# Kernel optimization log

Hardware: AMD Instinct MI355X
Metric: run time of the kernel (lower is better)

Reference implementation:

```python
import jax, jax.numpy as jnp
import numpy as np

N, M, D, O = 16384, 4096, 256, 256

def setup_inputs() -> dict:
    key = jax.random.key(0)
    k1, k2, k3, k4, k5, k6, k7 = jax.random.split(key, 7)
    H_fine = jax.random.normal(k1, (N, D), dtype=jnp.float32)
    H_coarse = jax.random.normal(k2, (M, D), dtype=jnp.float32)
    inter_channel_adj = jax.random.randint(k3, (N, M), 0, 2).astype(jnp.float32)
    # attention = nn.Linear(2D, 1): weight vector [2D], bias scalar
    wa = jax.random.normal(k4, (2 * D,), dtype=jnp.float32) * (1.0 / np.sqrt(2 * D))
    ba = jax.random.normal(k5, (1,), dtype=jnp.float32) * 0.01
    # transform = nn.Linear(D, O), xavier_uniform weight
    lim = np.sqrt(6.0 / (D + O)).astype(np.float32)
    Wt = jax.random.uniform(k6, (O, D), minval=-lim, maxval=lim, dtype=jnp.float32)
    bt = jax.random.normal(k7, (O,), dtype=jnp.float32) * 0.01
    return {"H_fine": H_fine, "H_coarse": H_coarse,
            "inter_channel_adj": inter_channel_adj,
            "wa": wa, "ba": ba, "Wt": Wt, "bt": bt}

def reference(H_fine, H_coarse, inter_channel_adj, wa, ba, Wt, bt):
    d = H_fine.shape[-1]
    # additive attention: score_ij = [hf_i ; hc_j] . wa + b
    # = hf_i . wa[:d] + hc_j . wa[d:] + b  (avoids [N,M,2D] concat)
    sf = H_fine @ wa[:d]            # [N]
    sc = H_coarse @ wa[d:]          # [M]
    scores = sf[:, None] + sc[None, :] + ba[0]        # [N, M]
    masked = scores * inter_channel_adj               # [N, M]
    weights = jax.nn.softmax(masked, axis=-1)         # [N, M]
    attn_out = weights @ H_coarse                     # [N, D]
    attn_out = attn_out + H_fine                      # add_self=True
    out = attn_out @ Wt.T + bt                        # [N, O]
    return jax.nn.relu(out)
```

## Files before the change

kernel.cpp:

```cpp
#include <hip/hip_runtime.h>
#include <hip/hip_fp16.h>
#include <stdint.h>

#define N_ 16384
#define M_ 4096
#define D_ 256
#define O_ 256

#define WS_T    0
#define WS_U    65536
#define WS_R    81920
#define WS_WTP  98304
#define WS_BP   229376

typedef float  f32x4  __attribute__((ext_vector_type(4)));
typedef _Float16 half8 __attribute__((ext_vector_type(8)));

__device__ __forceinline__ unsigned short f2h(float f) {
  __half h = __float2half(f);
  unsigned short u;
  __builtin_memcpy(&u, &h, 2);
  return u;
}
__device__ __forceinline__ uint32_t hpack(float a, float b) {
  __half2 h = __floats2half2_rn(a, b);
  uint32_t u;
  __builtin_memcpy(&u, &h, 4);
  return u;
}

__global__ __launch_bounds__(256) void prep_kernel(
    const float* __restrict__ Hf, const float* __restrict__ Hc,
    const float* __restrict__ wa, const float* __restrict__ ba,
    const float* __restrict__ Wt, float* __restrict__ tv,
    float* __restrict__ uv, unsigned short* __restrict__ BP,
    unsigned short* __restrict__ WtP, float* __restrict__ Rv) {
  __shared__ float tile[64][65];
  __shared__ float red[4][64];
  int b = blockIdx.x;
  int t = threadIdx.x;
  if (b < 5120) {
    int wv = t >> 6, lane = t & 63;
    const float* X; const float* w; const float* bias; float* outv; int row;
    if (b < 4096) { X = Hf; w = wa;      bias = ba;      outv = tv; row = b * 4 + wv; }
    else          { X = Hc; w = wa + D_; bias = nullptr; outv = uv; row = (b - 4096) * 4 + wv; }
    const float4* x4 = (const float4*)(X + (size_t)row * D_);
    const float4* w4 = (const float4*)w;
    float4 xa = x4[lane], wa4 = w4[lane];
    float s = xa.x * wa4.x + xa.y * wa4.y + xa.z * wa4.z + xa.w * wa4.w;
#pragma unroll
    for (int off = 32; off > 0; off >>= 1) s += __shfl_xor(s, off);
    if (lane == 0) outv[row] = expf(s + (bias ? bias[0] : 0.0f));
  } else if (b < 5376) {
    int bb = b - 5120;
    int bk = bb >> 2;
    int bc = bb & 3;
    int k0 = bk * 64, col0 = bc * 64;
    int lane = t & 63, wv = t >> 6;
    int m = lane & 15, q = lane >> 4;
    float colsum = 0.0f;
#pragma unroll
    for (int i = 0; i < 16; ++i) {
      int e = t + 256 * i;
      int kk = e >> 6, cc = e & 63;
      float v = Hc[(size_t)(k0 + kk) * D_ + col0 + cc];
      tile[kk][cc] = v;
      colsum += v;
    }
    red[wv][t & 63] = colsum;
    __syncthreads();
    if (t < 64)
      atomicAdd(&Rv[col0 + t], red[0][t] + red[1][t] + red[2][t] + red[3][t]);
#pragma unroll
    for (int t8 = 0; t8 < 2; ++t8) {
      int tile_id = t8 * 4 + wv;
      int sub = tile_id >> 2, g = tile_id & 3;
      int kgg = bk * 2 + sub;
      int cgg = bc * 4 + g;
      unsigned short v8[8];
#pragma unroll
      for (int j = 0; j < 8; ++j)
        v8[j] = f2h(tile[sub * 32 + q * 8 + j][g * 16 + m]);
      *(uint4*)(BP + ((size_t)(kgg * 16 + cgg) * 64 + lane) * 8) = *(uint4*)v8;
    }
  } else {
    int tt = (b - 5376) * 256 + t;
    int lane = tt & 63, cg = (tt >> 6) & 15, kg = tt >> 10;
    int m = lane & 15, q = lane >> 4;
    const float* src = Wt + (size_t)(cg * 16 + m) * D_ + kg * 32 + q * 8;
    float4 w0 = *(const float4*)src, w1 = *(const float4*)(src + 4);
    unsigned short v8[8];
    v8[0] = f2h(w0.x); v8[1] = f2h(w0.y); v8[2] = f2h(w0.z); v8[3] = f2h(w0.w);
    v8[4] = f2h(w1.x); v8[5] = f2h(w1.y); v8[6] = f2h(w1.z); v8[7] = f2h(w1.w);
    *(uint4*)(WtP + (size_t)tt * 8) = *(uint4*)v8;
  }
}

__device__ __forceinline__ half8 frag_f16(uint32_t bits, __half2 th,
                                          const __half2* up, __half2 mone) {
  union { half8 h; uint32_t u[4]; } r;
#pragma unroll
  for (int p = 0; p < 4; ++p) {
    __half2 v = __hfma2(th, up[p], mone);
    uint32_t c;
    __builtin_memcpy(&c, &v, 4);
    uint32_t mlo = (uint32_t)((int32_t)(bits << (31 - 2 * p)) >> 31);
    uint32_t mhi = (uint32_t)((int32_t)(bits << (30 - 2 * p)) >> 31);
    r.u[p] = c & ((mlo & 0x0000FFFFu) | (mhi & 0xFFFF0000u));
  }
  return r.h;
}

#define COMPUTE_K(WB0, WB1, KK, BUF)                                          \
  {                                                                           \
    uint4 uu = *(const uint4*)&u_h2[(KK) * 16 + q * 4];                       \
    __half2 up[4];                                                            \
    __builtin_memcpy(up, &uu, 16);                                            \
    half8 af = frag_f16(((WB0) >> sh) & 0xffu, th0, up, mone);                \
    _Pragma("unroll")                                                         \
    for (int n = 0; n < 4; ++n)                                               \
      acc[0][n] = __builtin_amdgcn_mfma_f32_16x16x32_f16(af, BUF[n], acc[0][n], 0, 0, 0); \
    af = frag_f16(((WB1) >> sh) & 0xffu, th1, up, mone);                      \
    _Pragma("unroll")                                                         \
    for (int n = 0; n < 4; ++n)                                               \
      acc[1][n] = __builtin_amdgcn_mfma_f32_16x16x32_f16(af, BUF[n], acc[1][n], 0, 0, 0); \
  }

__global__ __launch_bounds__(512, 4) void mega_kernel(
    const float* __restrict__ adj, const unsigned short* __restrict__ BP,
    const float* __restrict__ tv, const float* __restrict__ uv,
    const float* __restrict__ Rv, const float* __restrict__ Hf,
    const unsigned short* __restrict__ WtP, const float* __restrict__ bt,
    float* __restrict__ out) {
  __shared__ __align__(16) char smem[74880];
  unsigned int (*bt2)[132] = (unsigned int (*)[132])(smem);
  float* u_lds = (float*)(smem + 16896);
  uint32_t* u_h2 = (uint32_t*)(smem + 33280);
  float (*Cred)[260] = (float (*)[260])(smem + 41472);
  float* Lsum_lds = (float*)(smem + 74752);
  unsigned short (*attn)[264] = (unsigned short (*)[264])(smem);

  int tid = threadIdx.x;
  int w = tid >> 6, lane = tid & 63;
  int q = lane >> 4, m = lane & 15;
  int colq = w >> 1, ksub = w & 1;
  int i0 = blockIdx.x * 32;

  for (int i = tid; i < M_ / 2; i += 512) {
    float2 u2 = *(const float2*)(uv + 2 * i);
    u_lds[2 * i] = u2.x; u_lds[2 * i + 1] = u2.y;
    u_h2[i] = hpack(u2.x, u2.y);
  }
  __syncthreads();

  {
    int r0 = w * 4;
    const float* ar = adj + ((size_t)i0 + r0) * M_;
    float su[4] = {0.f, 0.f, 0.f, 0.f}, sc[4] = {0.f, 0.f, 0.f, 0.f};
    float a[4][4], na[4][4];
#pragma unroll
    for (int j = 0; j < 4; ++j)
#pragma unroll
      for (int c = 0; c < 4; ++c)
        a[j][c] = ar[(size_t)j * M_ + c * 64 + lane];
#pragma unroll 1
    for (int i = 0; i < 16; ++i) {
      int k0 = i * 256;
      int k1 = (i + 1 < 16) ? k0 + 256 : 0;
#pragma unroll
      for (int j = 0; j < 4; ++j)
#pragma unroll
        for (int c = 0; c < 4; ++c)
          na[j][c] = ar[(size_t)j * M_ + k1 + c * 64 + lane];
      unsigned long long bal[4][4];
#pragma unroll
      for (int j = 0; j < 4; ++j) {
#pragma unroll
        for (int c = 0; c < 4; ++c) {
          bal[j][c] = __ballot(a[j][c] != 0.0f);
          su[j] = fmaf(a[j][c], u_lds[k0 + c * 64 + lane], su[j]);
        }
        sc[j] += (a[j][0] + a[j][1]) + (a[j][2] + a[j][3]);
      }
      if (lane < 32) {
        int rowsel = lane >> 3;
        int c = (lane >> 1) & 3, hi = lane & 1;
        unsigned long long v0 = (c == 0) ? bal[0][0] : (c == 1) ? bal[0][1] : (c == 2) ? bal[0][2] : bal[0][3];
        unsigned long long v1 = (c == 0) ? bal[1][0] : (c == 1) ? bal[1][1] : (c == 2) ? bal[1][2] : bal[1][3];
        unsigned long long v2 = (c == 0) ? bal[2][0] : (c == 1) ? bal[2][1] : (c == 2) ? bal[2][2] : bal[2][3];
        unsigned long long v3 = (c == 0) ? bal[3][0] : (c == 1) ? bal[3][1] : (c == 2) ? bal[3][2] : bal[3][3];
        unsigned long long v = (rowsel == 0) ? v0 : (rowsel == 1) ? v1 : (rowsel == 2) ? v2 : v3;
        bt2[r0 + rowsel][i * 8 + c * 2 + hi] =
            hi ? (unsigned int)(v >> 32) : (unsigned int)v;
      }
#pragma unroll
      for (int j = 0; j < 4; ++j)
#pragma unroll
        for (int c = 0; c < 4; ++c) a[j][c] = na[j][c];
    }
#pragma unroll
    for (int off = 32; off > 0; off >>= 1) {
#pragma unroll
      for (int j = 0; j < 4; ++j) {
        su[j] += __shfl_xor(su[j], off);
        sc[j] += __shfl_xor(sc[j], off);
      }
    }
    if (lane == 0) {
#pragma unroll
      for (int j = 0; j < 4; ++j)
        Lsum_lds[r0 + j] = tv[i0 + r0 + j] * su[j] - sc[j];
    }
  }

  const unsigned short* bbase = BP + (size_t)(colq * 4) * 512 + (size_t)lane * 8;
  int kg0 = ksub * 64;
  half8 bufA[4], bufB[4];
#pragma unroll
  for (int n = 0; n < 4; ++n)
    bufA[n] = *(const half8*)(bbase + ((size_t)kg0 * 16 + n) * 512);

  __half2 th0 = __float2half2_rn(tv[i0 + m]);
  __half2 th1 = __float2half2_rn(tv[i0 + 16 + m]);
  const __half2 mone = __float2half2_rn(-1.0f);

  f32x4 acc[2][4];
#pragma unroll
  for (int s = 0; s < 2; ++s)
#pragma unroll
    for (int n = 0; n < 4; ++n) acc[s][n] = (f32x4){0.f, 0.f, 0.f, 0.f};

  __syncthreads();

#pragma unroll 1
  for (int it2 = 0; it2 < 32; ++it2) {
    int kg = kg0 + it2 * 2;
    uint2 W0 = *(const uint2*)&bt2[m][kg];
    uint2 W1 = *(const uint2*)&bt2[16 + m][kg];
    int sh = q * 8;

#pragma unroll
    for (int n = 0; n < 4; ++n)
      bufB[n] = *(const half8*)(bbase + ((size_t)(kg + 1) * 16 + n) * 512);
    COMPUTE_K(W0.x, W1.x, kg, bufA)

    int kn = (it2 + 1 < 32) ? kg + 2 : kg0;
#pragma unroll
    for (int n = 0; n < 4; ++n)
      bufA[n] = *(const half8*)(bbase + ((size_t)kn * 16 + n) * 512);
    COMPUTE_K(W0.y, W1.y, kg + 1, bufB)
  }

#pragma unroll
  for (int s4 = 0; s4 < 2; ++s4) {
    if (ksub == s4) {
#pragma unroll
      for (int s = 0; s < 2; ++s)
#pragma unroll
        for (int n = 0; n < 4; ++n) {
          int col = colq * 64 + n * 16 + m;
#pragma unroll
          for (int r = 0; r < 4; ++r) {
            int rl = s * 16 + q * 4 + r;
            if (s4 == 0) Cred[rl][col] = acc[s][n][r];
            else         Cred[rl][col] += acc[s][n][r];
          }
        }
    }
    __syncthreads();
  }

  {
    int row = tid >> 4;
    int c0 = (tid & 15) * 16;
    size_t grow = (size_t)i0 + row;
    float invL = 1.0f / (Lsum_lds[row] + (float)M_);
    const float* hfp = Hf + grow * D_ + c0;
    const float* rvp = Rv + c0;
    const float* crp = &Cred[row][c0];
#pragma unroll
    for (int g = 0; g < 4; ++g) {
      float4 cv = *(const float4*)(crp + g * 4);
      float4 rv = *(const float4*)(rvp + g * 4);
      float4 hv = *(const float4*)(hfp + g * 4);
      float v0 = fmaf(cv.x + rv.x, invL, hv.x);
      float v1 = fmaf(cv.y + rv.y, invL, hv.y);
      float v2 = fmaf(cv.z + rv.z, invL, hv.z);
      float v3 = fmaf(cv.w + rv.w, invL, hv.w);
      *(uint32_t*)&attn[row][c0 + g * 4]     = hpack(v0, v1);
      *(uint32_t*)&attn[row][c0 + g * 4 + 2] = hpack(v2, v3);
    }
  }
  __syncthreads();

  {
    int rt = w & 1, cq = w >> 1;
    f32x4 facc[4];
#pragma unroll
    for (int n = 0; n < 4; ++n) facc[n] = (f32x4){0.f, 0.f, 0.f, 0.f};
    const unsigned short* wwave = WtP + (size_t)(cq * 4) * 512 + (size_t)lane * 8;
#pragma unroll
    for (int kf = 0; kf < 8; ++kf) {
      half8 af = *(const half8*)&attn[rt * 16 + m][kf * 32 + q * 8];
#pragma unroll
      for (int n = 0; n < 4; ++n) {
        half8 bf = *(const half8*)(wwave + ((size_t)kf * 16 + n) * 512);
        facc[n] = __builtin_amdgcn_mfma_f32_16x16x32_f16(af, bf, facc[n], 0, 0, 0);
      }
    }
#pragma unroll
    for (int n = 0; n < 4; ++n) {
      int col = cq * 64 + n * 16 + m;
      float b = bt[col];
#pragma unroll
      for (int r = 0; r < 4; ++r) {
        size_t row = (size_t)i0 + rt * 16 + q * 4 + r;
        out[row * O_ + col] = fmaxf(facc[n][r] + b, 0.0f);
      }
    }
  }
}

extern "C" void kernel_launch(void* const* d_in, const int* in_sizes, int n_in,
                              void* d_out, int out_size, void* d_ws, size_t ws_size,
                              hipStream_t stream) {
  const float* Hf  = (const float*)d_in[0];
  const float* Hc  = (const float*)d_in[1];
  const float* adj = (const float*)d_in[2];
  const float* wa  = (const float*)d_in[3];
  const float* ba  = (const float*)d_in[4];
  const float* Wt  = (const float*)d_in[5];
  const float* bt  = (const float*)d_in[6];
  float* out = (float*)d_out;

  char* ws = (char*)d_ws;
  float* tv   = (float*)(ws + WS_T);
  float* uv   = (float*)(ws + WS_U);
  float* Rv   = (float*)(ws + WS_R);
  unsigned short* WtP = (unsigned short*)(ws + WS_WTP);
  unsigned short* BP  = (unsigned short*)(ws + WS_BP);

  hipMemsetAsync(Rv, 0, D_ * sizeof(float), stream);

  prep_kernel<<<5408, 256, 0, stream>>>(Hf, Hc, wa, ba, Wt, tv, uv, BP, WtP, Rv);
  mega_kernel<<<512, 512, 0, stream>>>(adj, BP, tv, uv, Rv, Hf, WtP, bt, out);
}
```

Baseline: 441.5 us.

## Interleave adjacency bitmask streaming with MFMA chunks via double-buffered LDS bits

The adjacency scan and the masked MFMA accumulation used to run as two phases: all mask bits went to LDS first, then the GEMM ran. They now run as one 16-chunk software pipeline. Each iteration loads and ballots the next 256-column chunk of adj into a double-buffered LDS bitmask while computing MFMAs on the current chunk. The wave work split also changes: each wave now owns one 16-row tile and 8 column groups, with a K-split over 2 halves, instead of 2 row tiles and 4 column groups. This is meant to hide the HBM-bound adj read behind tensor-core work and to shrink LDS use. In exchange it adds a block-wide barrier per chunk and raises register pressure from 8 B fragments loaded per k-step.

Measured after the change: 430.9 us. -2.4%, faster.

```diff
diff --git a/kernel.cpp b/kernel.cpp
--- a/kernel.cpp
+++ b/kernel.cpp
@@ -111,19 +111,72 @@
   return r.h;
 }
 
-#define COMPUTE_K(WB0, WB1, KK, BUF)                                          \
+#define LOADS(KB)                                                             \
+  _Pragma("unroll")                                                           \
+  for (int cc = 0; cc < 4; ++cc) {                                            \
+    na0[cc] = ar[(size_t)0 * M_ + (KB) + cc * 64 + lane];                     \
+    na1[cc] = ar[(size_t)1 * M_ + (KB) + cc * 64 + lane];                     \
+    na2[cc] = ar[(size_t)2 * M_ + (KB) + cc * 64 + lane];                     \
+    na3[cc] = ar[(size_t)3 * M_ + (KB) + cc * 64 + lane];                     \
+  }
+
+#define TAIL(BUF, KB)                                                         \
   {                                                                           \
-    uint4 uu = *(const uint4*)&u_h2[(KK) * 16 + q * 4];                       \
+    unsigned long long bal0[4], bal1[4], bal2[4], bal3[4];                    \
+    _Pragma("unroll")                                                         \
+    for (int cc = 0; cc < 4; ++cc) {                                          \
+      float uvv = u_lds[(KB) + cc * 64 + lane];                               \
+      bal0[cc] = __ballot(na0[cc] != 0.0f);                                   \
+      bal1[cc] = __ballot(na1[cc] != 0.0f);                                   \
+      bal2[cc] = __ballot(na2[cc] != 0.0f);                                   \
+      bal3[cc] = __ballot(na3[cc] != 0.0f);                                   \
+      su[0] = fmaf(na0[cc], uvv, su[0]);                                      \
+      su[1] = fmaf(na1[cc], uvv, su[1]);                                      \
+      su[2] = fmaf(na2[cc], uvv, su[2]);                                      \
+      su[3] = fmaf(na3[cc], uvv, su[3]);                                      \
+    }                                                                         \
+    sc[0] += (na0[0] + na0[1]) + (na0[2] + na0[3]);                           \
+    sc[1] += (na1[0] + na1[1]) + (na1[2] + na1[3]);                           \
+    sc[2] += (na2[0] + na2[1]) + (na2[2] + na2[3]);                           \
+    sc[3] += (na3[0] + na3[1]) + (na3[2] + na3[3]);                           \
+    if (lane < 32) {                                                          \
+      int rowsel = lane >> 3, ccs = (lane >> 1) & 3, hi = lane & 1;           \
+      unsigned long long v0 = ccs == 0 ? bal0[0] : ccs == 1 ? bal0[1] : ccs == 2 ? bal0[2] : bal0[3]; \
+      unsigned long long v1 = ccs == 0 ? bal1[0] : ccs == 1 ? bal1[1] : ccs == 2 ? bal1[2] : bal1[3]; \
+      unsigned long long v2 = ccs == 0 ? bal2[0] : ccs == 1 ? bal2[1] : ccs == 2 ? bal2[2] : bal2[3]; \
+      unsigned long long v3 = ccs == 0 ? bal3[0] : ccs == 1 ? bal3[1] : ccs == 2 ? bal3[2] : bal3[3]; \
+      unsigned long long v = rowsel == 0 ? v0 : rowsel == 1 ? v1 : rowsel == 2 ? v2 : v3; \
+      bits_lds[BUF][w * 4 + rowsel][ccs * 2 + hi] =                           \
+          hi ? (unsigned int)(v >> 32) : (unsigned int)v;                     \
+    }                                                                         \
+  }
+
+#define COMPUTE(C, BUF)                                                       \
+  _Pragma("unroll")                                                           \
+  for (int kk = 0; kk < 4; ++kk) {                                            \
+    int kgc = ks * 4 + kk, kg = (C) * 8 + kgc;                                \
+    uint32_t b32 = bits_lds[BUF][rt * 16 + m][kgc];                           \
+    uint4 uu = *(const uint4*)&u_h2[kg * 16 + q * 4];                         \
+    const unsigned short* bp = BP + ((size_t)(kg * 16 + cgh * 8)) * 512 + (size_t)lane * 8; \
+    half8 bf0 = *(const half8*)(bp);                                          \
+    half8 bf1 = *(const half8*)(bp + 512);                                    \
+    half8 bf2 = *(const half8*)(bp + 1024);                                   \
+    half8 bf3 = *(const half8*)(bp + 1536);                                   \
+    half8 bf4 = *(const half8*)(bp + 2048);                                   \
+    half8 bf5 = *(const half8*)(bp + 2560);                                   \
+    half8 bf6 = *(const half8*)(bp + 3072);                                   \
+    half8 bf7 = *(const half8*)(bp + 3584);                                   \
     __half2 up[4];                                                            \
     __builtin_memcpy(up, &uu, 16);                                            \
-    half8 af = frag_f16(((WB0) >> sh) & 0xffu, th0, up, mone);                \
-    _Pragma("unroll")                                                         \
-    for (int n = 0; n < 4; ++n)                                               \
-      acc[0][n] = __builtin_amdgcn_mfma_f32_16x16x32_f16(af, BUF[n], acc[0][n], 0, 0, 0); \
-    af = frag_f16(((WB1) >> sh) & 0xffu, th1, up, mone);                      \
-    _Pragma("unroll")                                                         \
-    for (int n = 0; n < 4; ++n)                                               \
-      acc[1][n] = __builtin_amdgcn_mfma_f32_16x16x32_f16(af, BUF[n], acc[1][n], 0, 0, 0); \
+    half8 af = frag_f16((b32 >> sh) & 0xffu, th, up, mone);                   \
+    acc[0] = __builtin_amdgcn_mfma_f32_16x16x32_f16(af, bf0, acc[0], 0, 0, 0); \
+    acc[1] = __builtin_amdgcn_mfma_f32_16x16x32_f16(af, bf1, acc[1], 0, 0, 0); \
+    acc[2] = __builtin_amdgcn_mfma_f32_16x16x32_f16(af, bf2, acc[2], 0, 0, 0); \
+    acc[3] = __builtin_amdgcn_mfma_f32_16x16x32_f16(af, bf3, acc[3], 0, 0, 0); \
+    acc[4] = __builtin_amdgcn_mfma_f32_16x16x32_f16(af, bf4, acc[4], 0, 0, 0); \
+    acc[5] = __builtin_amdgcn_mfma_f32_16x16x32_f16(af, bf5, acc[5], 0, 0, 0); \
+    acc[6] = __builtin_amdgcn_mfma_f32_16x16x32_f16(af, bf6, acc[6], 0, 0, 0); \
+    acc[7] = __builtin_amdgcn_mfma_f32_16x16x32_f16(af, bf7, acc[7], 0, 0, 0); \
   }
 
 __global__ __launch_bounds__(512, 4) void mega_kernel(
@@ -132,140 +185,78 @@
     const float* __restrict__ Rv, const float* __restrict__ Hf,
     const unsigned short* __restrict__ WtP, const float* __restrict__ bt,
     float* __restrict__ out) {
-  __shared__ __align__(16) char smem[74880];
-  unsigned int (*bt2)[132] = (unsigned int (*)[132])(smem);
-  float* u_lds = (float*)(smem + 16896);
-  uint32_t* u_h2 = (uint32_t*)(smem + 33280);
-  float (*Cred)[260] = (float (*)[260])(smem + 41472);
-  float* Lsum_lds = (float*)(smem + 74752);
+  __shared__ __align__(16) char smem[60288];
+  unsigned int (*bits_lds)[32][9] = (unsigned int (*)[32][9])(smem);
+  float* u_lds = (float*)(smem + 2304);
+  uint32_t* u_h2 = (uint32_t*)(smem + 18688);
+  float (*Cred)[260] = (float (*)[260])(smem + 26880);
+  float* Lsum_lds = (float*)(smem + 60160);
   unsigned short (*attn)[264] = (unsigned short (*)[264])(smem);
 
   int tid = threadIdx.x;
   int w = tid >> 6, lane = tid & 63;
   int q = lane >> 4, m = lane & 15;
-  int colq = w >> 1, ksub = w & 1;
+  int rt = w & 1, cgh = (w >> 1) & 1, ks = w >> 2;
+  int sh = q * 8;
   int i0 = blockIdx.x * 32;
+
+  const float* ar = adj + ((size_t)i0 + w * 4) * M_;
+  float su[4] = {0.f, 0.f, 0.f, 0.f}, sc[4] = {0.f, 0.f, 0.f, 0.f};
+  float na0[4], na1[4], na2[4], na3[4];
+
+  LOADS(0)
 
   for (int i = tid; i < M_ / 2; i += 512) {
     float2 u2 = *(const float2*)(uv + 2 * i);
     u_lds[2 * i] = u2.x; u_lds[2 * i + 1] = u2.y;
     u_h2[i] = hpack(u2.x, u2.y);
   }
+
+  __half2 th = __float2half2_rn(tv[i0 + rt * 16 + m]);
+  const __half2 mone = __float2half2_rn(-1.0f);
+
+  f32x4 acc[8];
+#pragma unroll
+  for (int n = 0; n < 8; ++n) acc[n] = (f32x4){0.f, 0.f, 0.f, 0.f};
+
   __syncthreads();
-
-  {
-    int r0 = w * 4;
-    const float* ar = adj + ((size_t)i0 + r0) * M_;
-    float su[4] = {0.f, 0.f, 0.f, 0.f}, sc[4] = {0.f, 0.f, 0.f, 0.f};
-    float a[4][4], na[4][4];
+  TAIL(0, 0)
+  __syncthreads();
+
+#pragma unroll 1
+  for (int c = 0; c < 16; ++c) {
+    if (c < 15) { LOADS((c + 1) * 256) }
+    COMPUTE(c, c & 1)
+    if (c < 15) { TAIL((c + 1) & 1, (c + 1) * 256) }
+    __syncthreads();
+  }
+
+#pragma unroll
+  for (int off = 32; off > 0; off >>= 1) {
+    su[0] += __shfl_xor(su[0], off); sc[0] += __shfl_xor(sc[0], off);
+    su[1] += __shfl_xor(su[1], off); sc[1] += __shfl_xor(sc[1], off);
+    su[2] += __shfl_xor(su[2], off); sc[2] += __shfl_xor(sc[2], off);
+    su[3] += __shfl_xor(su[3], off); sc[3] += __shfl_xor(sc[3], off);
+  }
+  if (lane == 0) {
 #pragma unroll
     for (int j = 0; j < 4; ++j)
-#pragma unroll
-      for (int c = 0; c < 4; ++c)
-        a[j][c] = ar[(size_t)j * M_ + c * 64 + lane];
-#pragma unroll 1
-    for (int i = 0; i < 16; ++i) {
-      int k0 = i * 256;
-      int k1 = (i + 1 < 16) ? k0 + 256 : 0;
-#pragma unroll
-      for (int j = 0; j < 4; ++j)
-#pragma unroll
-        for (int c = 0; c < 4; ++c)
-          na[j][c] = ar[(size_t)j * M_ + k1 + c * 64 + lane];
-      unsigned long long bal[4][4];
-#pragma unroll
-      for (int j = 0; j < 4; ++j) {
-#pragma unroll
-        for (int c = 0; c < 4; ++c) {
-          bal[j][c] = __ballot(a[j][c] != 0.0f);
-          su[j] = fmaf(a[j][c], u_lds[k0 + c * 64 + lane], su[j]);
+      Lsum_lds[w * 4 + j] = tv[i0 + w * 4 + j] * su[j] - sc[j];
+  }
+
+#pragma unroll
+  for (int s4 = 0; s4 < 2; ++s4) {
+    if (ks == s4) {
+#pragma unroll
+      for (int g = 0; g < 8; ++g) {
+        int col = (cgh * 8 + g) * 16 + m;
+#pragma unroll
+        for (int r = 0; r < 4; ++r) {
+          int rl = rt * 16 + q * 4 + r;
+          if (s4 == 0) Cred[rl][col] = acc[g][r];
+          else         Cred[rl][col] += acc[g][r];
         }
-        sc[j] += (a[j][0] + a[j][1]) + (a[j][2] + a[j][3]);
       }
-      if (lane < 32) {
-        int rowsel = lane >> 3;
-        int c = (lane >> 1) & 3, hi = lane & 1;
-        unsigned long long v0 = (c == 0) ? bal[0][0] : (c == 1) ? bal[0][1] : (c == 2) ? bal[0][2] : bal[0][3];
-        unsigned long long v1 = (c == 0) ? bal[1][0] : (c == 1) ? bal[1][1] : (c == 2) ? bal[1][2] : bal[1][3];
-        unsigned long long v2 = (c == 0) ? bal[2][0] : (c == 1) ? bal[2][1] : (c == 2) ? bal[2][2] : bal[2][3];
-        unsigned long long v3 = (c == 0) ? bal[3][0] : (c == 1) ? bal[3][1] : (c == 2) ? bal[3][2] : bal[3][3];
-        unsigned long long v = (rowsel == 0) ? v0 : (rowsel == 1) ? v1 : (rowsel == 2) ? v2 : v3;
-        bt2[r0 + rowsel][i * 8 + c * 2 + hi] =
-            hi ? (unsigned int)(v >> 32) : (unsigned int)v;
-      }
-#pragma unroll
-      for (int j = 0; j < 4; ++j)
-#pragma unroll
-        for (int c = 0; c < 4; ++c) a[j][c] = na[j][c];
-    }
-#pragma unroll
-    for (int off = 32; off > 0; off >>= 1) {
-#pragma unroll
-      for (int j = 0; j < 4; ++j) {
-        su[j] += __shfl_xor(su[j], off);
-        sc[j] += __shfl_xor(sc[j], off);
-      }
-    }
-    if (lane == 0) {
-#pragma unroll
-      for (int j = 0; j < 4; ++j)
-        Lsum_lds[r0 + j] = tv[i0 + r0 + j] * su[j] - sc[j];
-    }
-  }
-
-  const unsigned short* bbase = BP + (size_t)(colq * 4) * 512 + (size_t)lane * 8;
-  int kg0 = ksub * 64;
-  half8 bufA[4], bufB[4];
-#pragma unroll
-  for (int n = 0; n < 4; ++n)
-    bufA[n] = *(const half8*)(bbase + ((size_t)kg0 * 16 + n) * 512);
-
-  __half2 th0 = __float2half2_rn(tv[i0 + m]);
-  __half2 th1 = __float2half2_rn(tv[i0 + 16 + m]);
-  const __half2 mone = __float2half2_rn(-1.0f);
-
-  f32x4 acc[2][4];
-#pragma unroll
-  for (int s = 0; s < 2; ++s)
-#pragma unroll
-    for (int n = 0; n < 4; ++n) acc[s][n] = (f32x4){0.f, 0.f, 0.f, 0.f};
-
-  __syncthreads();
-
-#pragma unroll 1
-  for (int it2 = 0; it2 < 32; ++it2) {
-    int kg = kg0 + it2 * 2;
-    uint2 W0 = *(const uint2*)&bt2[m][kg];
-    uint2 W1 = *(const uint2*)&bt2[16 + m][kg];
-    int sh = q * 8;
-
-#pragma unroll
-    for (int n = 0; n < 4; ++n)
-      bufB[n] = *(const half8*)(bbase + ((size_t)(kg + 1) * 16 + n) * 512);
-    COMPUTE_K(W0.x, W1.x, kg, bufA)
-
-    int kn = (it2 + 1 < 32) ? kg + 2 : kg0;
-#pragma unroll
-    for (int n = 0; n < 4; ++n)
-      bufA[n] = *(const half8*)(bbase + ((size_t)kn * 16 + n) * 512);
-    COMPUTE_K(W0.y, W1.y, kg + 1, bufB)
-  }
-
-#pragma unroll
-  for (int s4 = 0; s4 < 2; ++s4) {
-    if (ksub == s4) {
-#pragma unroll
-      for (int s = 0; s < 2; ++s)
-#pragma unroll
-        for (int n = 0; n < 4; ++n) {
-          int col = colq * 64 + n * 16 + m;
-#pragma unroll
-          for (int r = 0; r < 4; ++r) {
-            int rl = s * 16 + q * 4 + r;
-            if (s4 == 0) Cred[rl][col] = acc[s][n][r];
-            else         Cred[rl][col] += acc[s][n][r];
-          }
-        }
     }
     __syncthreads();
   }
@@ -294,14 +285,14 @@
   __syncthreads();
 
   {
-    int rt = w & 1, cq = w >> 1;
+    int rt2 = w & 1, cq = w >> 1;
     f32x4 facc[4];
 #pragma unroll
     for (int n = 0; n < 4; ++n) facc[n] = (f32x4){0.f, 0.f, 0.f, 0.f};
     const unsigned short* wwave = WtP + (size_t)(cq * 4) * 512 + (size_t)lane * 8;
 #pragma unroll
     for (int kf = 0; kf < 8; ++kf) {
-      half8 af = *(const half8*)&attn[rt * 16 + m][kf * 32 + q * 8];
+      half8 af = *(const half8*)&attn[rt2 * 16 + m][kf * 32 + q * 8];
 #pragma unroll
       for (int n = 0; n < 4; ++n) {
         half8 bf = *(const half8*)(wwave + ((size_t)kf * 16 + n) * 512);
@@ -314,7 +305,7 @@
       float b = bt[col];
 #pragma unroll
       for (int r = 0; r < 4; ++r) {
-        size_t row = (size_t)i0 + rt * 16 + q * 4 + r;
+        size_t row = (size_t)i0 + rt2 * 16 + q * 4 + r;
         out[row * O_ + col] = fmaxf(facc[n][r] + b, 0.0f);
       }
     }
```
